# Optimization experiments

Hardware: AMD Instinct MI355X
Metric: run time of the kernel (lower is better)

Reference implementation:

```python
import jax, jax.numpy as jnp
import numpy as np

B, N, D, M, K, H = 8, 196, 512, 20, 77, 8
SPARSITY_RATIO = 0.1


def _ln(x, g, b, eps=1e-5):
    mu = x.mean(axis=-1, keepdims=True)
    var = ((x - mu) ** 2).mean(axis=-1, keepdims=True)
    return (x - mu) / jnp.sqrt(var + eps) * g + b


def setup_inputs() -> dict:
    key = jax.random.key(0)
    ks = jax.random.split(key, 8)
    s = lambda i, shape, sc=1.0: jax.random.normal(ks[i], shape, jnp.float32) * sc
    return {
        "F_clean": s(0, (B, N, D)),
        "text_features": s(1, (K, D)),
        "in_proj_w": s(2, (3 * D, D), 0.02),
        "in_proj_b": jnp.zeros((3 * D,), jnp.float32),
        "out_w": s(3, (D, D), 0.02),
        "out_b": jnp.zeros((D,), jnp.float32),
        "ln1_g": jnp.ones((D,), jnp.float32),
        "ln1_b": jnp.zeros((D,), jnp.float32),
        "ln2_g": jnp.ones((D,), jnp.float32),
        "ln2_b": jnp.zeros((D,), jnp.float32),
        "mlp_w1": s(4, (D, D), 0.02),
        "mlp_b1": jnp.zeros((D,), jnp.float32),
        "mlp_ln_g": jnp.ones((D,), jnp.float32),
        "mlp_ln_b": jnp.zeros((D,), jnp.float32),
        "mlp_w2": s(5, (M, D), 0.02),
        "mlp_b2": jnp.zeros((M,), jnp.float32),
        "templates": s(6, (M, D)),
    }


def reference(F_clean, text_features, in_proj_w, in_proj_b, out_w, out_b,
              ln1_g, ln1_b, ln2_g, ln2_b,
              mlp_w1, mlp_b1, mlp_ln_g, mlp_ln_b, mlp_w2, mlp_b2, templates):
    hd = D // H
    text_exp = jnp.broadcast_to(text_features[None], (B, K, D))
    q_in = _ln(text_exp, ln1_g, ln1_b)
    k_in = _ln(F_clean, ln1_g, ln1_b)
    Wq, Wk, Wv = in_proj_w[:D], in_proj_w[D:2 * D], in_proj_w[2 * D:]
    bq, bk, bv = in_proj_b[:D], in_proj_b[D:2 * D], in_proj_b[2 * D:]
    q = (q_in @ Wq.T + bq).reshape(B, K, H, hd).transpose(0, 2, 1, 3)
    k = (k_in @ Wk.T + bk).reshape(B, N, H, hd).transpose(0, 2, 1, 3)
    v = (F_clean @ Wv.T + bv).reshape(B, N, H, hd).transpose(0, 2, 1, 3)
    scores = jnp.einsum('bhkd,bhnd->bhkn', q, k) / jnp.sqrt(jnp.float32(hd))
    attn = jax.nn.softmax(scores, axis=-1)                     # [B,H,K,N]
    ctx = jnp.einsum('bhkn,bhnd->bhkd', attn, v)
    ctx = ctx.transpose(0, 2, 1, 3).reshape(B, K, D)
    attn_output = ctx @ out_w.T + out_b
    attn_weights = attn.mean(axis=1)                           # [B,K,N]
    attn_output = _ln(attn_output, ln2_g, ln2_b)

    # Vectorized form of the per-patch loop (j over N)
    w = attn_weights.transpose(0, 2, 1)[..., None]             # [B,N,K,1]
    interact = F_clean[:, :, None, :] * attn_output[:, None, :, :]  # [B,N,K,D]
    weighted = interact * w
    clean = weighted - weighted.mean(axis=2, keepdims=True)
    h = clean @ mlp_w1.T + mlp_b1
    h = _ln(h, mlp_ln_g, mlp_ln_b)
    h = jax.nn.gelu(h, approximate=False)
    comps = h @ mlp_w2.T + mlp_b2                              # [B,N,K,M]
    Q_patch = (comps * w).sum(axis=2)                          # [B,N,M]

    # Outer-product construct: [B,N,D,M]
    Q = F_clean[..., None] * templates.T[None, None] * Q_patch[:, :, None, :]

    # Top-k sparsify along D, then L2-normalize along D
    k_keep = max(int(D * SPARSITY_RATIO), 1)
    Qr = Q.transpose(0, 1, 3, 2).reshape(B * N * M, D)
    _, idx = jax.lax.top_k(jnp.abs(Qr), k_keep)
    rows = jnp.arange(B * N * M)[:, None]
    mask = jnp.zeros_like(Qr).at[rows, idx].set(1.0)
    Qs = (Qr * mask).reshape(B, N, M, D).transpose(0, 1, 3, 2)
    nrm = jnp.maximum(jnp.linalg.norm(Qs, axis=2, keepdims=True), 1e-6)
    return (Qs / nrm, attn_weights)
```

## Files before the change

### kernel.cpp

```cpp
#include <hip/hip_runtime.h>
#include <hip/hip_bf16.h>
#include <math.h>


typedef unsigned int uint;
typedef _Float16 f16x8 __attribute__((ext_vector_type(8)));
typedef float f32x4 __attribute__((ext_vector_type(4)));

#define DI __device__ __forceinline__

DI float wsumf(float v){ for(int o=32;o>0;o>>=1) v += __shfl_xor(v,o,64); return v; }
DI int   wsumi(int v){ for(int o=32;o>0;o>>=1) v += __shfl_xor(v,o,64); return v; }
DI float wmaxf(float v){ for(int o=32;o>0;o>>=1) v = fmaxf(v,__shfl_xor(v,o,64)); return v; }

__global__ __launch_bounds__(256) void k0_transpose(const float* ipw, const float* ow, const float* mw1,
                             float* WT, float* OWT, _Float16* w1hi, _Float16* w1lo){
  int bid = blockIdx.x;
  if(bid < 768){
    __shared__ float t[32][33];
    int tdin = bid & 15, tdout = bid >> 4;
    int tx = threadIdx.x & 31, ty = threadIdx.x >> 5;
    int dout0 = tdout*32, din0 = tdin*32;
    for(int r=ty; r<32; r+=8) t[r][tx] = ipw[(size_t)(dout0+r)*512 + din0+tx];
    __syncthreads();
    for(int r=ty; r<32; r+=8) WT[(size_t)(din0+r)*1536 + dout0+tx] = t[tx][r];
  } else if(bid < 1024){
    __shared__ float t[32][33];
    int b2 = bid - 768;
    int tdin = b2 & 15, tdout = b2 >> 4;
    int tx = threadIdx.x & 31, ty = threadIdx.x >> 5;
    int dout0 = tdout*32, din0 = tdin*32;
    for(int r=ty; r<32; r+=8) t[r][tx] = ow[(size_t)(dout0+r)*512 + din0+tx];
    __syncthreads();
    for(int r=ty; r<32; r+=8) OWT[(size_t)(din0+r)*512 + dout0+tx] = t[tx][r];
  } else {
    int i3 = (bid-1024)*256 + threadIdx.x;
    int t = i3&7, ln = (i3>>3)&63, J = (i3>>9)&31, T = i3>>14;
    int j = J*16 + (ln&15);
    int d = T*32 + ((ln>>4)<<3) + t;
    float w = mw1[j*512 + d] * 64.0f;
    _Float16 hi = (_Float16)w;
    _Float16 lo = (_Float16)(w - (float)hi);
    w1hi[i3] = hi; w1lo[i3] = lo;
  }
}

__global__ __launch_bounds__(256) void k1_q(const float* text, const float* ipb,
                                            const float* g1, const float* b1p,
                                            const float* WT, float* qws){
  int k = blockIdx.x >> 1, half = blockIdx.x & 1;
  int tid = threadIdx.x;
  __shared__ float xln[512];
  __shared__ float rA[4], rB[4];
  float x0 = text[k*512+tid], x1 = text[k*512+256+tid];
  float s1 = wsumf(x0+x1), s2 = wsumf(x0*x0+x1*x1);
  int w = tid>>6, ln = tid&63;
  if(!ln){ rA[w]=s1; rB[w]=s2; }
  __syncthreads();
  float mu = (rA[0]+rA[1]+rA[2]+rA[3])*(1.f/512.f);
  float var = (rB[0]+rB[1]+rB[2]+rB[3])*(1.f/512.f) - mu*mu;
  float rs = 1.f/sqrtf(fmaxf(var,0.f) + 1e-5f);
  xln[tid]     = (x0-mu)*rs*g1[tid]     + b1p[tid];
  xln[tid+256] = (x1-mu)*rs*g1[tid+256] + b1p[tid+256];
  __syncthreads();
  int d = half*256 + tid;
  float a0=0.f,a1=0.f,a2=0.f,a3=0.f;
  for(int din=0; din<512; din+=4){
    a0 += xln[din  ] * WT[(din  )*1536 + d];
    a1 += xln[din+1] * WT[(din+1)*1536 + d];
    a2 += xln[din+2] * WT[(din+2)*1536 + d];
    a3 += xln[din+3] * WT[(din+3)*1536 + d];
  }
  qws[k*512+d] = ipb[d] + ((a0+a1)+(a2+a3));
}

__global__ __launch_bounds__(512) void k2_kv(const float* F, const float* ipb,
                                             const float* g1, const float* b1p,
                                             const float* WT, float* kmat, float* vmat){
  int r0 = blockIdx.x*4; int tid = threadIdx.x;
  __shared__ float xs[4][512];
  __shared__ float xl[4][512];
  __shared__ float red[4][64];
  __shared__ float mu4[4], rs4[4];
  for(int e=tid; e<2048; e+=512){ int r=e>>9, d=e&511; xs[r][d] = F[(size_t)(r0+r)*512 + d]; }
  __syncthreads();
  {
    float s=0.f, q=0.f; int r=0, t=0;
    if(tid<256){
      r = tid>>6; t = tid&63;
      for(int i=0;i<8;++i){ float v = xs[r][t+64*i]; s+=v; q+=v*v; }
      red[r][t] = s;
    }
    __syncthreads();
    if(tid<4){ float ss=0; for(int i=0;i<64;++i) ss+=red[tid][i]; mu4[tid]=ss*(1.f/512.f); }
    __syncthreads();
    if(tid<256) red[r][t] = q;
    __syncthreads();
    if(tid<4){ float qq=0; for(int i=0;i<64;++i) qq+=red[tid][i];
      float m=mu4[tid]; rs4[tid]=1.f/sqrtf(fmaxf(qq*(1.f/512.f)-m*m,0.f)+1e-5f); }
    __syncthreads();
  }
  for(int e=tid; e<2048; e+=512){ int r=e>>9, d=e&511;
    xl[r][d] = (xs[r][d]-mu4[r])*rs4[r]*g1[d] + b1p[d]; }
  __syncthreads();
  int d=tid;
  float ak[4], av[4];
  float bk=ipb[512+d], bv=ipb[1024+d];
  #pragma unroll
  for(int r=0;r<4;++r){ ak[r]=bk; av[r]=bv; }
  for(int din=0; din<512; din+=4){
    float wk[4], wv[4];
    #pragma unroll
    for(int u=0;u<4;++u){ wk[u]=WT[(din+u)*1536+512+d]; wv[u]=WT[(din+u)*1536+1024+d]; }
    #pragma unroll
    for(int r=0;r<4;++r){
      float4 a4 = *(const float4*)&xl[r][din];
      float4 x4 = *(const float4*)&xs[r][din];
      ak[r] += a4.x*wk[0]+a4.y*wk[1]+a4.z*wk[2]+a4.w*wk[3];
      av[r] += x4.x*wv[0]+x4.y*wv[1]+x4.z*wv[2]+x4.w*wv[3];
    }
  }
  #pragma unroll
  for(int r=0;r<4;++r){
    size_t base = (size_t)(r0+r)*512;
    kmat[base+d]=ak[r]; vmat[base+d]=av[r];
  }
}

__global__ __launch_bounds__(256) void k3_attn(const float* qws, const float* kmat, float* attf){
  int bid = blockIdx.x;
  int kc = bid>>6, b = (bid>>3)&7, h = bid&7;
  int tid = threadIdx.x; int n = tid; int w = tid>>6, ln = tid&63;
  __shared__ float qb[8][64];
  __shared__ float rM[8][4], rS[8][4];
  float4 kr[16];
  if(n < 196){
    const float4* kp = (const float4*)(kmat + ((size_t)(b*196+n))*512 + h*64);
    #pragma unroll
    for(int j=0;j<16;++j) kr[j] = kp[j];
  }
  int kbase = kc*8;
  for(int e=tid; e<512; e+=256){ int kk=e>>6, j=e&63; int k=kbase+kk;
    qb[kk][j] = (k<77)? qws[k*512 + h*64 + j] : 0.f; }
  __syncthreads();
  float sc[8];
  #pragma unroll
  for(int kk=0;kk<8;++kk){
    float s = 0.f;
    if(n<196){
      const float4* q4 = (const float4*)qb[kk];
      #pragma unroll
      for(int j=0;j<16;++j){ float4 q = q4[j];
        s += q.x*kr[j].x + q.y*kr[j].y + q.z*kr[j].z + q.w*kr[j].w; }
      sc[kk] = s*0.125f;
    } else sc[kk] = -INFINITY;
  }
  #pragma unroll
  for(int kk=0;kk<8;++kk){ float m = wmaxf(sc[kk]); if(!ln) rM[kk][w]=m; }
  __syncthreads();
  float ex[8];
  #pragma unroll
  for(int kk=0;kk<8;++kk){
    float m = fmaxf(fmaxf(rM[kk][0],rM[kk][1]),fmaxf(rM[kk][2],rM[kk][3]));
    float e = expf(sc[kk]-m);
    ex[kk]=e;
    float s = wsumf(e); if(!ln) rS[kk][w]=s;
  }
  __syncthreads();
  #pragma unroll
  for(int kk=0;kk<8;++kk){
    int k = kbase+kk;
    if(k<77 && n<196){
      float tot = rS[kk][0]+rS[kk][1]+rS[kk][2]+rS[kk][3];
      attf[(((size_t)(b*8+h))*77 + k)*196 + n] = ex[kk]/tot;
    }
  }
}

__global__ __launch_bounds__(256) void k4_ctx(const float* attf, const float* vmat, float* ctx){
  int bid = blockIdx.x;
  int kc = bid>>6, b = (bid>>3)&7, h = bid&7;
  int tid = threadIdx.x; int ng = tid>>6, j = tid&63;
  __shared__ float vT[196][64];
  __shared__ float aT[8][196];
  __shared__ float red[8][4][64];
  for(int e=tid; e<196*16; e+=256){ int n=e>>4, jc=e&15;
    const float4* vp = (const float4*)(vmat + ((size_t)(b*196+n))*512 + h*64);
    *(float4*)&vT[n][jc*4] = vp[jc];
  }
  int kbase=kc*8;
  for(int e=tid; e<8*196; e+=256){ int kk=e/196, n=e-kk*196; int k=kbase+kk;
    aT[kk][n] = (k<77)? attf[(((size_t)(b*8+h))*77+k)*196+n] : 0.f; }
  __syncthreads();
  float vr[49];
  #pragma unroll
  for(int t=0;t<49;++t) vr[t] = vT[ng*49+t][j];
  #pragma unroll
  for(int kk=0;kk<8;++kk){
    float p=0.f;
    #pragma unroll
    for(int t=0;t<49;++t) p += aT[kk][ng*49+t]*vr[t];
    red[kk][ng][j]=p;
  }
  __syncthreads();
  for(int e=tid; e<512; e+=256){ int kk=e>>6, j2=e&63; int k=kbase+kk;
    if(k<77){
      float s = red[kk][0][j2]+red[kk][1][j2]+red[kk][2][j2]+red[kk][3][j2];
      ctx[((size_t)(b*77+k))*512 + h*64 + j2] = s;
    } }
}

__global__ void k5_attw(const float* attf, float* attw, float* out2){
  int idx = blockIdx.x*256+threadIdx.x;
  if(idx >= 8*77*196) return;
  int b = idx / (77*196); int rem = idx - b*(77*196);
  float s=0.f;
  #pragma unroll
  for(int h=0;h<8;++h) s += attf[((size_t)(b*8+h))*77*196 + rem];
  s *= 0.125f;
  attw[idx]=s; out2[idx]=s;
}

__global__ __launch_bounds__(512) void k6_ao(const float* ctx, const float* OWT,
                                             const float* ob, const float* g2, const float* b2p,
                                             float* AO){
  int R0 = blockIdx.x*4; int tid = threadIdx.x;
  __shared__ float xs[4][512];
  __shared__ float ao[4][512];
  __shared__ float red[4][64];
  __shared__ float mu4[4], rs4[4];
  for(int e=tid;e<2048;e+=512){ int r=e>>9,d=e&511; xs[r][d]=ctx[(size_t)(R0+r)*512+d]; }
  __syncthreads();
  int d=tid;
  float a[4]; float obv=ob[d];
  #pragma unroll
  for(int r=0;r<4;++r) a[r]=obv;
  for(int din=0;din<512;din+=4){
    float wv[4];
    #pragma unroll
    for(int u=0;u<4;++u) wv[u]=OWT[(din+u)*512+d];
    #pragma unroll
    for(int r=0;r<4;++r){
      float4 x4 = *(const float4*)&xs[r][din];
      a[r] += x4.x*wv[0]+x4.y*wv[1]+x4.z*wv[2]+x4.w*wv[3];
    }
  }
  #pragma unroll
  for(int r=0;r<4;++r) ao[r][d]=a[r];
  __syncthreads();
  {
    float s=0.f,q=0.f; int r=0,t=0;
    if(tid<256){
      r=tid>>6; t=tid&63;
      for(int i=0;i<8;++i){ float v=ao[r][t+64*i]; s+=v; q+=v*v; }
      red[r][t]=s;
    }
    __syncthreads();
    if(tid<4){ float ss=0; for(int i=0;i<64;++i) ss+=red[tid][i]; mu4[tid]=ss*(1.f/512.f); }
    __syncthreads();
    if(tid<256) red[r][t]=q;
    __syncthreads();
    if(tid<4){ float qq=0; for(int i=0;i<64;++i) qq+=red[tid][i];
      float m=mu4[tid]; rs4[tid]=1.f/sqrtf(fmaxf(qq*(1.f/512.f)-m*m,0.f)+1e-5f); }
    __syncthreads();
  }
  for(int e=tid;e<2048;e+=512){ int r=e>>9,dd=e&511;
    AO[(size_t)(R0+r)*512+dd] = (ao[r][dd]-mu4[r])*rs4[r]*g2[dd] + b2p[dd]; }
}

__global__ __launch_bounds__(512) void k6b_sv(const float* AO, const float* attw,
                                              float* Svws, float* wsumws){
  int bid = blockIdx.x;
  int b = bid/25, nt = bid - b*25;
  int n0 = nt*8;
  int tid = threadIdx.x;
  __shared__ float wsK[80][8];
  for(int e=tid; e<640; e+=512){ int k=e>>3, r=e&7; int n=n0+r;
    wsK[k][r] = (k<77 && n<196)? attw[((size_t)(b*77+k))*196 + n] : 0.f; }
  __syncthreads();
  if(tid<8){ int n=n0+tid;
    if(n<196){ float s=0.f;
      for(int k=0;k<77;++k) s+=wsK[k][tid];
      wsumws[b*196+n]=s; } }
  int d = tid;
  float acc[8];
  #pragma unroll
  for(int r=0;r<8;++r) acc[r]=0.f;
  const float* aob = AO + (size_t)b*77*512 + d;
  for(int k=0;k<77;++k){
    float a = aob[(size_t)k*512];
    #pragma unroll
    for(int r=0;r<8;++r) acc[r] += wsK[k][r]*a;
  }
  #pragma unroll
  for(int r=0;r<8;++r){ int n=n0+r; if(n<196)
    Svws[((size_t)(b*196+n))*512 + d] = acc[r]*(1.f/77.f); }
}

struct __align__(16) K7Smem {
  _Float16 Ah[16*512];
  _Float16 Al[16*512];
  float b1s[512], gs[512], bs[512];
  float wvS[80];
  float redS[8][16], redQ[8][16];
  float muA[16], rsA[16];
  float gfin[512];
  float qred[320];
};

#define K7_MFMA3(ACC, AFH, AFL, BH, BL) \
  ACC = __builtin_amdgcn_mfma_f32_16x16x32_f16(AFL, BH, ACC, 0,0,0); \
  ACC = __builtin_amdgcn_mfma_f32_16x16x32_f16(AFH, BL, ACC, 0,0,0); \
  ACC = __builtin_amdgcn_mfma_f32_16x16x32_f16(AFH, BH, ACC, 0,0,0);

struct Bset { f16x8 h0,h1,h2,h3,l0,l1,l2,l3; };

DI void loadB(Bset& s, const _Float16* bph, const _Float16* bpl, int t){
  const _Float16* ph = bph + t*16384;
  const _Float16* pl = bpl + t*16384;
  s.h0 = *(const f16x8*)(ph);       s.h1 = *(const f16x8*)(ph+512);
  s.h2 = *(const f16x8*)(ph+1024);  s.h3 = *(const f16x8*)(ph+1536);
  s.l0 = *(const f16x8*)(pl);       s.l1 = *(const f16x8*)(pl+512);
  s.l2 = *(const f16x8*)(pl+1024);  s.l3 = *(const f16x8*)(pl+1536);
}

DI void stepMFMA1(f32x4 acc[4], const _Float16* Ah, const _Float16* Al,
                  const Bset& B, int t, int ln){
  int off = t*512 + ((ln + t)&63)*8;
  f16x8 fh = *(const f16x8*)&Ah[off];
  f16x8 fl = *(const f16x8*)&Al[off];
  K7_MFMA3(acc[0], fh, fl, B.h0, B.l0)
  K7_MFMA3(acc[1], fh, fl, B.h1, B.l1)
  K7_MFMA3(acc[2], fh, fl, B.h2, B.l2)
  K7_MFMA3(acc[3], fh, fl, B.h3, B.l3)
}

template<int K0>
DI void k7_body(int bn, const float* F, const float* AO, const float* attw,
                const _Float16* w1hi, const _Float16* w1lo,
                const float* b1p, const float* lng, const float* lnb,
                const float* w2, const float* b2p,
                const float* Svws, const float* wsumws,
                float* Qpws, K7Smem& sm){
  int b = bn/196, n = bn - b*196;
  int tid = threadIdx.x; int w = tid>>6, ln = tid&63;
  int col = ln&15, quad = ln>>4;
  const float* AObase = AO + (size_t)b*77*512;
  sm.b1s[tid] = b1p[tid]; sm.gs[tid] = lng[tid]; sm.bs[tid] = lnb[tid];
  if(tid<80) sm.wvS[tid] = (tid<77)? attw[((size_t)(b*77+tid))*196+n] : 0.f;
  __syncthreads();

  {
    int d0 = (tid&63)*8;
    int r0 = tid>>6;
    int t  = d0>>5;
    int k8 = (d0&31)>>3;
    float4 f0 = *(const float4*)&F[(size_t)bn*512 + d0];
    float4 f1 = *(const float4*)&F[(size_t)bn*512 + d0+4];
    float4 sv0 = *(const float4*)&Svws[(size_t)bn*512 + d0];
    float4 sv1 = *(const float4*)&Svws[(size_t)bn*512 + d0+4];
    float fk[8] = {f0.x*1024.f,f0.y*1024.f,f0.z*1024.f,f0.w*1024.f,
                   f1.x*1024.f,f1.y*1024.f,f1.z*1024.f,f1.w*1024.f};
    float sv[8] = {sv0.x,sv0.y,sv0.z,sv0.w,sv1.x,sv1.y,sv1.z,sv1.w};
    #pragma unroll
    for(int it=0; it<2; ++it){
      int row = r0 + it*8;
      int grow = K0 + row;
      bool ok = grow < 77;
      int rl = ok ? grow : 0;
      float wm = ok ? sm.wvS[grow] : 0.f;
      const float* ap = AObase + (size_t)rl*512 + d0;
      float4 a0 = *(const float4*)ap;
      float4 a1 = *(const float4*)(ap+4);
      float av[8] = {a0.x,a0.y,a0.z,a0.w,a1.x,a1.y,a1.z,a1.w};
      f16x8 hfrag, lfrag;
      #pragma unroll
      for(int i=0;i<8;++i){
        float c = ok ? fk[i]*(wm*av[i] - sv[i]) : 0.f;
        _Float16 h = (_Float16)c;
        hfrag[i] = h;
        lfrag[i] = (_Float16)(c - (float)h);
      }
      int lane = row | (k8<<4);
      int pos = (lane + t)&63;
      int idx = t*512 + pos*8;
      *(f16x8*)&sm.Ah[idx] = hfrag;
      *(f16x8*)&sm.Al[idx] = lfrag;
    }
  }
  __syncthreads();
  f32x4 acc[4];
  #pragma unroll
  for(int jj=0;jj<4;++jj) acc[jj] = (f32x4){0.f,0.f,0.f,0.f};

  const _Float16* bph = w1hi + ((w*4)*64 + ln)*8;
  const _Float16* bpl = w1lo + ((w*4)*64 + ln)*8;

  Bset s0, s1;
  loadB(s0, bph, bpl, 0);
  #pragma unroll 1
  for(int tt=0; tt<16; tt+=2){
    loadB(s1, bph, bpl, tt+1);
    stepMFMA1(acc, sm.Ah, sm.Al, s0, tt, ln);
    if(tt+2<16) loadB(s0, bph, bpl, tt+2);
    stepMFMA1(acc, sm.Ah, sm.Al, s1, tt+1, ln);
  }

  const float UNS = 1.f/65536.f;
  {
    float s[4]={0.f,0.f,0.f,0.f}, q[4]={0.f,0.f,0.f,0.f};
    #pragma unroll
    for(int jj=0;jj<4;++jj){
      int j = w*64 + jj*16 + col; float bj = sm.b1s[j];
      #pragma unroll
      for(int r=0;r<4;++r){
        float h = acc[jj][r]*UNS + bj;
        s[r]+=h; q[r]+=h*h;
      }
    }
    #pragma unroll
    for(int r=0;r<4;++r){
      #pragma unroll
      for(int o=1;o<16;o<<=1){ s[r]+=__shfl_xor(s[r],o,64); q[r]+=__shfl_xor(q[r],o,64); }
    }
    if(col==0){
      #pragma unroll
      for(int r=0;r<4;++r){ int row = quad*4+r; sm.redS[w][row]=s[r]; sm.redQ[w][row]=q[r]; }
    }
  }
  __syncthreads();
  if(tid<16){
    float s=0.f,q=0.f;
    #pragma unroll
    for(int ww=0;ww<8;++ww){ s+=sm.redS[ww][tid]; q+=sm.redQ[ww][tid]; }
    float mu = s*(1.f/512.f);
    float var = q*(1.f/512.f)-mu*mu;
    sm.muA[tid]=mu; sm.rsA[tid]=1.f/sqrtf(fmaxf(var,0.f)+1e-5f);
  }
  __syncthreads();
  float gp[4]={0.f,0.f,0.f,0.f};
  #pragma unroll
  for(int r=0;r<4;++r){
    int lr = quad*4+r;
    float mu=sm.muA[lr], rs=sm.rsA[lr], wk=sm.wvS[K0+lr];
    #pragma unroll
    for(int jj=0;jj<4;++jj){
      int j = w*64 + jj*16 + col;
      float h = acc[jj][r]*UNS + sm.b1s[j];
      float x = (h-mu)*rs;
      float y = x*sm.gs[j]+sm.bs[j];
      float gl = 0.5f*y*(1.f+erff(y*0.70710678118654752f));
      gp[jj] += wk*gl;
    }
  }
  #pragma unroll
  for(int jj=0;jj<4;++jj){ gp[jj]+=__shfl_xor(gp[jj],16,64); gp[jj]+=__shfl_xor(gp[jj],32,64); }
  if(ln<16){
    #pragma unroll
    for(int jj=0;jj<4;++jj) sm.gfin[w*64 + jj*16 + ln] = gp[jj];
  }
  __syncthreads();
  if(tid<320){ int m=tid>>4, seg=tid&15; float p=0.f;
    for(int u=0;u<32;++u){ int uu=(u+seg)&31; int j=seg*32+uu;
      p += sm.gfin[j]*w2[m*512+j]; }
    sm.qred[m*16+seg]=p; }
  __syncthreads();
  if(tid<20){ float s=0.f;
    for(int seg=0;seg<16;++seg) s+=sm.qred[tid*16+seg];
    if(K0==0) s += b2p[tid]*wsumws[bn];
    Qpws[(size_t)bn*100 + (K0>>4)*20 + tid]=s; }
}

__global__
__attribute__((amdgpu_flat_work_group_size(512,512)))
void k7_mlp(const float* F, const float* AO, const float* attw,
            const _Float16* w1hi, const _Float16* w1lo,
            const float* b1p, const float* lng, const float* lnb,
            const float* w2, const float* b2p,
            const float* Svws, const float* wsumws,
            float* Qpws){
  __shared__ K7Smem sm;
  int bid = blockIdx.x;
  int bn = bid/5;
  int c = bid - bn*5;
  switch(c){
    case 0: k7_body<0 >(bn,F,AO,attw,w1hi,w1lo,b1p,lng,lnb,w2,b2p,Svws,wsumws,Qpws,sm); break;
    case 1: k7_body<16>(bn,F,AO,attw,w1hi,w1lo,b1p,lng,lnb,w2,b2p,Svws,wsumws,Qpws,sm); break;
    case 2: k7_body<32>(bn,F,AO,attw,w1hi,w1lo,b1p,lng,lnb,w2,b2p,Svws,wsumws,Qpws,sm); break;
    case 3: k7_body<48>(bn,F,AO,attw,w1hi,w1lo,b1p,lng,lnb,w2,b2p,Svws,wsumws,Qpws,sm); break;
    default:k7_body<64>(bn,F,AO,attw,w1hi,w1lo,b1p,lng,lnb,w2,b2p,Svws,wsumws,Qpws,sm); break;
  }
}

__global__ __launch_bounds__(256) void k8_topk(const float* F, const float* T,
                                               const float* Qpws, float* out1){
  int bn = blockIdx.x; int tid = threadIdx.x;
  int w = tid>>6, ln = tid&63;
  __shared__ float Fv[512];
  __shared__ float QpS[20];
  __shared__ float ninv[20];
  __shared__ unsigned char selb[20][64];
  for(int e=tid;e<512;e+=256) Fv[e]=F[(size_t)bn*512+e];
  if(tid<20){
    const float* qp = Qpws + (size_t)bn*100 + tid;
    QpS[tid] = qp[0]+qp[20]+qp[40]+qp[60]+qp[80];
  }
  __syncthreads();
  for(int rr=0; rr<5; ++rr){
    int m = rr*4 + w;
    float qv[8]; uint key[8];
    const float4* tp = (const float4*)(T + (size_t)m*512 + ln*8);
    float4 t0 = tp[0], t1 = tp[1];
    float tf[8] = {t0.x,t0.y,t0.z,t0.w,t1.x,t1.y,t1.z,t1.w};
    float qp = QpS[m];
    #pragma unroll
    for(int i=0;i<8;++i){ float p = Fv[ln*8+i]*tf[i]; qv[i]=p*qp;
      key[i]=__float_as_uint(qv[i])&0x7fffffffu; }
    uint th=0u;
    for(int bit=30; bit>=0; --bit){
      uint cand = th | (1u<<bit);
      int c=0;
      #pragma unroll
      for(int i=0;i<8;++i) c += (int)__popcll(__ballot(key[i]>=cand));
      if(c>=51) th=cand;
    }
    int cg=0;
    #pragma unroll
    for(int i=0;i<8;++i) cg += (int)__popcll(__ballot(key[i]>th));
    int rneed = 51-cg;
    int eqc=0;
    #pragma unroll
    for(int i=0;i<8;++i) eqc += (key[i]==th);
    int pre=eqc;
    for(int o=1;o<64;o<<=1){ int v=__shfl_up(pre,o,64); if(ln>=o) pre+=v; }
    pre -= eqc;
    unsigned char mbits=0; float ss=0.f; int rk=pre;
    #pragma unroll
    for(int i=0;i<8;++i){
      bool s;
      if(key[i]>th) s=true;
      else if(key[i]==th){ s = (rk<rneed); rk++; }
      else s=false;
      if(s){ mbits |= (unsigned char)(1u<<i); ss += qv[i]*qv[i]; }
    }
    ss = wsumf(ss);
    if(ln==0) ninv[m] = 1.f/fmaxf(sqrtf(ss),1e-6f);
    selb[m][ln]=mbits;
  }
  __syncthreads();
  size_t base=(size_t)bn*10240;
  for(int e=tid;e<10240;e+=256){
    int d=e/20, mm=e-d*20;
    float val=0.f;
    if((selb[mm][d>>3]>>(d&7))&1){
      val = Fv[d]*T[(size_t)mm*512+d]*QpS[mm]*ninv[mm];
    }
    out1[base+e]=val;
  }
}

extern "C" void kernel_launch(void* const* d_in, const int* in_sizes, int n_in,
                              void* d_out, int out_size, void* d_ws, size_t ws_size,
                              hipStream_t stream){
  const float* F    = (const float*)d_in[0];
  const float* text = (const float*)d_in[1];
  const float* ipw  = (const float*)d_in[2];
  const float* ipb  = (const float*)d_in[3];
  const float* outw = (const float*)d_in[4];
  const float* outb = (const float*)d_in[5];
  const float* g1   = (const float*)d_in[6];
  const float* b1   = (const float*)d_in[7];
  const float* g2   = (const float*)d_in[8];
  const float* b2   = (const float*)d_in[9];
  const float* mw1  = (const float*)d_in[10];
  const float* mb1  = (const float*)d_in[11];
  const float* mlg  = (const float*)d_in[12];
  const float* mlb  = (const float*)d_in[13];
  const float* mw2  = (const float*)d_in[14];
  const float* mb2  = (const float*)d_in[15];
  const float* tmpl = (const float*)d_in[16];
  float* ws = (float*)d_ws;
  float* WT   = ws;
  float* OWT  = ws +  786432;
  float* qws  = ws + 1048576;
  float* kmat = ws + 1088000;
  float* vmat = ws + 1890816;
  float* attf = ws + 2693632;
  float* attw = ws + 3659520;
  float* ctx  = ws + 3780256;
  float* AO   = ws + 4095648;
  _Float16* w1hi = (_Float16*)(ws + 4473760);
  _Float16* w1lo = (_Float16*)(ws + 4604832);
  float* wsum = ws + 1048576;
  float* Sv   = ws + 1088000;
  float* Qp   = ws +  786432;
  float* out1 = (float*)d_out;
  float* out2 = out1 + 16056320;

  hipLaunchKernelGGL(k0_transpose, dim3(2048), dim3(256), 0, stream, ipw, outw, mw1, WT, OWT, w1hi, w1lo);
  hipLaunchKernelGGL(k1_q,   dim3(154), dim3(256), 0, stream, text, ipb, g1, b1, WT, qws);
  hipLaunchKernelGGL(k2_kv,  dim3(392), dim3(512), 0, stream, F, ipb, g1, b1, WT, kmat, vmat);
  hipLaunchKernelGGL(k3_attn,dim3(640), dim3(256), 0, stream, qws, kmat, attf);
  hipLaunchKernelGGL(k4_ctx, dim3(640), dim3(256), 0, stream, attf, vmat, ctx);
  hipLaunchKernelGGL(k5_attw,dim3(472), dim3(256), 0, stream, attf, attw, out2);
  hipLaunchKernelGGL(k6_ao,  dim3(154), dim3(512), 0, stream, ctx, OWT, outb, g2, b2, AO);
  hipLaunchKernelGGL(k6b_sv, dim3(200), dim3(512), 0, stream, AO, attw, Sv, wsum);
  hipLaunchKernelGGL(k7_mlp, dim3(7840),dim3(512), 0, stream, F, AO, attw, w1hi, w1lo, mb1, mlg, mlb, mw2, mb2, Sv, wsum, Qp);
  hipLaunchKernelGGL(k8_topk,dim3(1568),dim3(256), 0, stream, F, tmpl, Qp, out1);
}
```

Before: 710.0 us.

## Process two patches per k7 block to reuse W1 fragments across MFMA tiles

Each k7_mlp block now handles a pair of (b,n) patches instead of one, keeping two 16-row A tiles in shared memory and reusing every loaded W1 hi/lo B fragment for both tiles. The grid is halved, which cuts global/L2 traffic for the W1 weights per unit of work and amortises the per-block parameter loads. In exchange, shared memory and accumulator register usage roughly double, which may lower occupancy.

```diff
diff --git a/kernel.cpp b/kernel.cpp
--- a/kernel.cpp
+++ b/kernel.cpp
@@ -298,14 +298,14 @@
 }
 
 struct __align__(16) K7Smem {
-  _Float16 Ah[16*512];
-  _Float16 Al[16*512];
+  _Float16 Ah[2*16*512];
+  _Float16 Al[2*16*512];
   float b1s[512], gs[512], bs[512];
-  float wvS[80];
-  float redS[8][16], redQ[8][16];
-  float muA[16], rsA[16];
-  float gfin[512];
-  float qred[320];
+  float wvS[2][80];
+  float redS[8][32], redQ[8][32];
+  float muA[32], rsA[32];
+  float gfin[2][512];
+  float qred[2][320];
 };
 
 #define K7_MFMA3(ACC, AFH, AFL, BH, BL) \
@@ -324,30 +324,36 @@
   s.l2 = *(const f16x8*)(pl+1024);  s.l3 = *(const f16x8*)(pl+1536);
 }
 
-DI void stepMFMA1(f32x4 acc[4], const _Float16* Ah, const _Float16* Al,
+DI void stepMFMA2(f32x4 acc[2][4], const _Float16* Ah, const _Float16* Al,
                   const Bset& B, int t, int ln){
-  int off = t*512 + ((ln + t)&63)*8;
-  f16x8 fh = *(const f16x8*)&Ah[off];
-  f16x8 fl = *(const f16x8*)&Al[off];
-  K7_MFMA3(acc[0], fh, fl, B.h0, B.l0)
-  K7_MFMA3(acc[1], fh, fl, B.h1, B.l1)
-  K7_MFMA3(acc[2], fh, fl, B.h2, B.l2)
-  K7_MFMA3(acc[3], fh, fl, B.h3, B.l3)
+  #pragma unroll
+  for(int s=0; s<2; ++s){
+    int off = (s*16 + t)*512 + ((ln + t)&63)*8;
+    f16x8 fh = *(const f16x8*)&Ah[off];
+    f16x8 fl = *(const f16x8*)&Al[off];
+    K7_MFMA3(acc[s][0], fh, fl, B.h0, B.l0)
+    K7_MFMA3(acc[s][1], fh, fl, B.h1, B.l1)
+    K7_MFMA3(acc[s][2], fh, fl, B.h2, B.l2)
+    K7_MFMA3(acc[s][3], fh, fl, B.h3, B.l3)
+  }
 }
 
 template<int K0>
-DI void k7_body(int bn, const float* F, const float* AO, const float* attw,
+DI void k7_body(int pair, const float* F, const float* AO, const float* attw,
                 const _Float16* w1hi, const _Float16* w1lo,
                 const float* b1p, const float* lng, const float* lnb,
                 const float* w2, const float* b2p,
                 const float* Svws, const float* wsumws,
                 float* Qpws, K7Smem& sm){
-  int b = bn/196, n = bn - b*196;
+  int bn0 = pair*2, bn1 = pair*2+1;
+  int b0 = bn0/196, n0 = bn0 - b0*196;
+  int b1c = bn1/196, n1 = bn1 - b1c*196;
   int tid = threadIdx.x; int w = tid>>6, ln = tid&63;
   int col = ln&15, quad = ln>>4;
-  const float* AObase = AO + (size_t)b*77*512;
   sm.b1s[tid] = b1p[tid]; sm.gs[tid] = lng[tid]; sm.bs[tid] = lnb[tid];
-  if(tid<80) sm.wvS[tid] = (tid<77)? attw[((size_t)(b*77+tid))*196+n] : 0.f;
+  if(tid<160){ int s = tid/80, k = tid - s*80;
+    int bb = s? b1c:b0, nn = s? n1:n0;
+    sm.wvS[s][k] = (k<77)? attw[((size_t)(bb*77+k))*196+nn] : 0.f; }
   __syncthreads();
 
   {
@@ -355,43 +361,50 @@
     int r0 = tid>>6;
     int t  = d0>>5;
     int k8 = (d0&31)>>3;
-    float4 f0 = *(const float4*)&F[(size_t)bn*512 + d0];
-    float4 f1 = *(const float4*)&F[(size_t)bn*512 + d0+4];
-    float4 sv0 = *(const float4*)&Svws[(size_t)bn*512 + d0];
-    float4 sv1 = *(const float4*)&Svws[(size_t)bn*512 + d0+4];
-    float fk[8] = {f0.x*1024.f,f0.y*1024.f,f0.z*1024.f,f0.w*1024.f,
-                   f1.x*1024.f,f1.y*1024.f,f1.z*1024.f,f1.w*1024.f};
-    float sv[8] = {sv0.x,sv0.y,sv0.z,sv0.w,sv1.x,sv1.y,sv1.z,sv1.w};
-    #pragma unroll
-    for(int it=0; it<2; ++it){
-      int row = r0 + it*8;
-      int grow = K0 + row;
-      bool ok = grow < 77;
-      int rl = ok ? grow : 0;
-      float wm = ok ? sm.wvS[grow] : 0.f;
-      const float* ap = AObase + (size_t)rl*512 + d0;
-      float4 a0 = *(const float4*)ap;
-      float4 a1 = *(const float4*)(ap+4);
-      float av[8] = {a0.x,a0.y,a0.z,a0.w,a1.x,a1.y,a1.z,a1.w};
-      f16x8 hfrag, lfrag;
-      #pragma unroll
-      for(int i=0;i<8;++i){
-        float c = ok ? fk[i]*(wm*av[i] - sv[i]) : 0.f;
-        _Float16 h = (_Float16)c;
-        hfrag[i] = h;
-        lfrag[i] = (_Float16)(c - (float)h);
+    #pragma unroll
+    for(int s=0; s<2; ++s){
+      int bn = s? bn1:bn0;
+      const float* AObase = AO + (size_t)(s? b1c:b0)*77*512;
+      float4 f0 = *(const float4*)&F[(size_t)bn*512 + d0];
+      float4 f1 = *(const float4*)&F[(size_t)bn*512 + d0+4];
+      float4 sv0 = *(const float4*)&Svws[(size_t)bn*512 + d0];
+      float4 sv1 = *(const float4*)&Svws[(size_t)bn*512 + d0+4];
+      float fk[8] = {f0.x*1024.f,f0.y*1024.f,f0.z*1024.f,f0.w*1024.f,
+                     f1.x*1024.f,f1.y*1024.f,f1.z*1024.f,f1.w*1024.f};
+      float sv[8] = {sv0.x,sv0.y,sv0.z,sv0.w,sv1.x,sv1.y,sv1.z,sv1.w};
+      #pragma unroll
+      for(int it=0; it<2; ++it){
+        int row = r0 + it*8;
+        int grow = K0 + row;
+        bool ok = grow < 77;
+        int rl = ok ? grow : 0;
+        float wm = ok ? sm.wvS[s][grow] : 0.f;
+        const float* ap = AObase + (size_t)rl*512 + d0;
+        float4 a0 = *(const float4*)ap;
+        float4 a1 = *(const float4*)(ap+4);
+        float av[8] = {a0.x,a0.y,a0.z,a0.w,a1.x,a1.y,a1.z,a1.w};
+        f16x8 hfrag, lfrag;
+        #pragma unroll
+        for(int i=0;i<8;++i){
+          float c = ok ? fk[i]*(wm*av[i] - sv[i]) : 0.f;
+          _Float16 h = (_Float16)c;
+          hfrag[i] = h;
+          lfrag[i] = (_Float16)(c - (float)h);
+        }
+        int lane = row | (k8<<4);
+        int pos = (lane + t)&63;
+        int idx = ((s*16 + t)*512) + pos*8;
+        *(f16x8*)&sm.Ah[idx] = hfrag;
+        *(f16x8*)&sm.Al[idx] = lfrag;
       }
-      int lane = row | (k8<<4);
-      int pos = (lane + t)&63;
-      int idx = t*512 + pos*8;
-      *(f16x8*)&sm.Ah[idx] = hfrag;
-      *(f16x8*)&sm.Al[idx] = lfrag;
-    }
-  }
-  __syncthreads();
-  f32x4 acc[4];
-  #pragma unroll
-  for(int jj=0;jj<4;++jj) acc[jj] = (f32x4){0.f,0.f,0.f,0.f};
+    }
+  }
+  __syncthreads();
+  f32x4 acc[2][4];
+  #pragma unroll
+  for(int s=0;s<2;++s)
+    #pragma unroll
+    for(int jj=0;jj<4;++jj) acc[s][jj] = (f32x4){0.f,0.f,0.f,0.f};
 
   const _Float16* bph = w1hi + ((w*4)*64 + ln)*8;
   const _Float16* bpl = w1lo + ((w*4)*64 + ln)*8;
@@ -401,35 +414,36 @@
   #pragma unroll 1
   for(int tt=0; tt<16; tt+=2){
     loadB(s1, bph, bpl, tt+1);
-    stepMFMA1(acc, sm.Ah, sm.Al, s0, tt, ln);
+    stepMFMA2(acc, sm.Ah, sm.Al, s0, tt, ln);
     if(tt+2<16) loadB(s0, bph, bpl, tt+2);
-    stepMFMA1(acc, sm.Ah, sm.Al, s1, tt+1, ln);
+    stepMFMA2(acc, sm.Ah, sm.Al, s1, tt+1, ln);
   }
 
   const float UNS = 1.f/65536.f;
-  {
-    float s[4]={0.f,0.f,0.f,0.f}, q[4]={0.f,0.f,0.f,0.f};
+  #pragma unroll
+  for(int s=0;s<2;++s){
+    float sv4[4]={0.f,0.f,0.f,0.f}, q[4]={0.f,0.f,0.f,0.f};
     #pragma unroll
     for(int jj=0;jj<4;++jj){
       int j = w*64 + jj*16 + col; float bj = sm.b1s[j];
       #pragma unroll
       for(int r=0;r<4;++r){
-        float h = acc[jj][r]*UNS + bj;
-        s[r]+=h; q[r]+=h*h;
+        float h = acc[s][jj][r]*UNS + bj;
+        sv4[r]+=h; q[r]+=h*h;
       }
     }
     #pragma unroll
     for(int r=0;r<4;++r){
       #pragma unroll
-      for(int o=1;o<16;o<<=1){ s[r]+=__shfl_xor(s[r],o,64); q[r]+=__shfl_xor(q[r],o,64); }
+      for(int o=1;o<16;o<<=1){ sv4[r]+=__shfl_xor(sv4[r],o,64); q[r]+=__shfl_xor(q[r],o,64); }
     }
     if(col==0){
       #pragma unroll
-      for(int r=0;r<4;++r){ int row = quad*4+r; sm.redS[w][row]=s[r]; sm.redQ[w][row]=q[r]; }
-    }
-  }
-  __syncthreads();
-  if(tid<16){
+      for(int r=0;r<4;++r){ int row = s*16+quad*4+r; sm.redS[w][row]=sv4[r]; sm.redQ[w][row]=q[r]; }
+    }
+  }
+  __syncthreads();
+  if(tid<32){
     float s=0.f,q=0.f;
     #pragma unroll
     for(int ww=0;ww<8;++ww){ s+=sm.redS[ww][tid]; q+=sm.redQ[ww][tid]; }
@@ -438,37 +452,48 @@
     sm.muA[tid]=mu; sm.rsA[tid]=1.f/sqrtf(fmaxf(var,0.f)+1e-5f);
   }
   __syncthreads();
-  float gp[4]={0.f,0.f,0.f,0.f};
-  #pragma unroll
-  for(int r=0;r<4;++r){
-    int lr = quad*4+r;
-    float mu=sm.muA[lr], rs=sm.rsA[lr], wk=sm.wvS[K0+lr];
-    #pragma unroll
-    for(int jj=0;jj<4;++jj){
-      int j = w*64 + jj*16 + col;
-      float h = acc[jj][r]*UNS + sm.b1s[j];
-      float x = (h-mu)*rs;
-      float y = x*sm.gs[j]+sm.bs[j];
-      float gl = 0.5f*y*(1.f+erff(y*0.70710678118654752f));
-      gp[jj] += wk*gl;
-    }
-  }
-  #pragma unroll
-  for(int jj=0;jj<4;++jj){ gp[jj]+=__shfl_xor(gp[jj],16,64); gp[jj]+=__shfl_xor(gp[jj],32,64); }
+  float gp[2][4] = {{0.f,0.f,0.f,0.f},{0.f,0.f,0.f,0.f}};
+  #pragma unroll
+  for(int s=0;s<2;++s){
+    #pragma unroll
+    for(int r=0;r<4;++r){
+      int lr = quad*4+r;
+      float mu=sm.muA[s*16+lr], rs=sm.rsA[s*16+lr], wk=sm.wvS[s][K0+lr];
+      #pragma unroll
+      for(int jj=0;jj<4;++jj){
+        int j = w*64 + jj*16 + col;
+        float h = acc[s][jj][r]*UNS + sm.b1s[j];
+        float x = (h-mu)*rs;
+        float y = x*sm.gs[j]+sm.bs[j];
+        float gl = 0.5f*y*(1.f+erff(y*0.70710678118654752f));
+        gp[s][jj] += wk*gl;
+      }
+    }
+  }
+  #pragma unroll
+  for(int s=0;s<2;++s)
+    #pragma unroll
+    for(int jj=0;jj<4;++jj){ gp[s][jj]+=__shfl_xor(gp[s][jj],16,64); gp[s][jj]+=__shfl_xor(gp[s][jj],32,64); }
   if(ln<16){
     #pragma unroll
-    for(int jj=0;jj<4;++jj) sm.gfin[w*64 + jj*16 + ln] = gp[jj];
-  }
-  __syncthreads();
-  if(tid<320){ int m=tid>>4, seg=tid&15; float p=0.f;
+    for(int s=0;s<2;++s)
+      #pragma unroll
+      for(int jj=0;jj<4;++jj) sm.gfin[s][w*64 + jj*16 + ln] = gp[s][jj];
+  }
+  __syncthreads();
+  for(int e=tid; e<640; e+=512){
+    int s = e/320, rem = e - s*320;
+    int m = rem>>4, seg = rem&15; float p=0.f;
     for(int u=0;u<32;++u){ int uu=(u+seg)&31; int j=seg*32+uu;
-      p += sm.gfin[j]*w2[m*512+j]; }
-    sm.qred[m*16+seg]=p; }
-  __syncthreads();
-  if(tid<20){ float s=0.f;
-    for(int seg=0;seg<16;++seg) s+=sm.qred[tid*16+seg];
-    if(K0==0) s += b2p[tid]*wsumws[bn];
-    Qpws[(size_t)bn*100 + (K0>>4)*20 + tid]=s; }
+      p += sm.gfin[s][j]*w2[m*512+j]; }
+    sm.qred[s][m*16+seg]=p;
+  }
+  __syncthreads();
+  if(tid<40){ int s=tid/20, m=tid-s*20; float acc2=0.f;
+    for(int seg=0;seg<16;++seg) acc2+=sm.qred[s][m*16+seg];
+    int bn = s? bn1:bn0;
+    if(K0==0) acc2 += b2p[m]*wsumws[bn];
+    Qpws[(size_t)bn*100 + (K0>>4)*20 + m]=acc2; }
 }
 
 __global__
@@ -481,14 +506,14 @@
             float* Qpws){
   __shared__ K7Smem sm;
   int bid = blockIdx.x;
-  int bn = bid/5;
-  int c = bid - bn*5;
+  int pair = bid/5;
+  int c = bid - pair*5;
   switch(c){
-    case 0: k7_body<0 >(bn,F,AO,attw,w1hi,w1lo,b1p,lng,lnb,w2,b2p,Svws,wsumws,Qpws,sm); break;
-    case 1: k7_body<16>(bn,F,AO,attw,w1hi,w1lo,b1p,lng,lnb,w2,b2p,Svws,wsumws,Qpws,sm); break;
-    case 2: k7_body<32>(bn,F,AO,attw,w1hi,w1lo,b1p,lng,lnb,w2,b2p,Svws,wsumws,Qpws,sm); break;
-    case 3: k7_body<48>(bn,F,AO,attw,w1hi,w1lo,b1p,lng,lnb,w2,b2p,Svws,wsumws,Qpws,sm); break;
-    default:k7_body<64>(bn,F,AO,attw,w1hi,w1lo,b1p,lng,lnb,w2,b2p,Svws,wsumws,Qpws,sm); break;
+    case 0: k7_body<0 >(pair,F,AO,attw,w1hi,w1lo,b1p,lng,lnb,w2,b2p,Svws,wsumws,Qpws,sm); break;
+    case 1: k7_body<16>(pair,F,AO,attw,w1hi,w1lo,b1p,lng,lnb,w2,b2p,Svws,wsumws,Qpws,sm); break;
+    case 2: k7_body<32>(pair,F,AO,attw,w1hi,w1lo,b1p,lng,lnb,w2,b2p,Svws,wsumws,Qpws,sm); break;
+    case 3: k7_body<48>(pair,F,AO,attw,w1hi,w1lo,b1p,lng,lnb,w2,b2p,Svws,wsumws,Qpws,sm); break;
+    default:k7_body<64>(pair,F,AO,attw,w1hi,w1lo,b1p,lng,lnb,w2,b2p,Svws,wsumws,Qpws,sm); break;
   }
 }
 
@@ -605,6 +630,6 @@
   hipLaunchKernelGGL(k5_attw,dim3(472), dim3(256), 0, stream, attf, attw, out2);
   hipLaunchKernelGGL(k6_ao,  dim3(154), dim3(512), 0, stream, ctx, OWT, outb, g2, b2, AO);
   hipLaunchKernelGGL(k6b_sv, dim3(200), dim3(512), 0, stream, AO, attw, Sv, wsum);
-  hipLaunchKernelGGL(k7_mlp, dim3(7840),dim3(512), 0, stream, F, AO, attw, w1hi, w1lo, mb1, mlg, mlb, mw2, mb2, Sv, wsum, Qp);
+  hipLaunchKernelGGL(k7_mlp, dim3(3920),dim3(512), 0, stream, F, AO, attw, w1hi, w1lo, mb1, mlg, mlb, mw2, mb2, Sv, wsum, Qp);
   hipLaunchKernelGGL(k8_topk,dim3(1568),dim3(256), 0, stream, F, tmpl, Qp, out1);
 }
```

Measured after the change: 580.2 us (median of 2 runs). -18.3%, faster.
